# Kernel optimization log

Hardware: AMD Instinct MI355X
Metric: run time of the kernel (lower is better)

The kernel has to match this reference:

```python
import jax, jax.numpy as jnp
import numpy as np

DIM = 512
W = 64            # windowSize
R = 128           # receptiveSize
H = 8             # numHeads
HD = 64           # headDim
MAXD = W - 1 + (R - W) // 2  # maxDisparity = 95


def setup_inputs() -> dict:
    key = jax.random.key(0)
    ks = jax.random.split(key, 12)
    B_ = 512
    inp = {
        'x':  jax.random.normal(ks[0], (B_, 1 + W, DIM), jnp.float32),
        'x_': jax.random.normal(ks[1], (B_, 1 + R, DIM), jnp.float32),
        'mask_left':  jax.random.randint(ks[2], (4, 1 + W, 1 + R), 0, 2, jnp.int32),
        'mask_right': jax.random.randint(ks[3], (4, 1 + W, 1 + R), 0, 2, jnp.int32),
        'nW': 64,
        'rel_table': jax.random.normal(ks[4], (2 * MAXD + 1, H), jnp.float32) * 0.02,
        'cls_self':  jax.random.normal(ks[5], (1, H, 1, 1), jnp.float32) * 0.02,
        'cls_up':    jax.random.normal(ks[6], (1, H, 1, R), jnp.float32) * 0.02,
        'cls_down':  jax.random.normal(ks[7], (1, H, W, 1), jnp.float32) * 0.02,
        'Wq':  jax.random.normal(ks[8], (H * HD, DIM), jnp.float32) * 0.02,
        'bq':  jnp.zeros((H * HD,), jnp.float32),
        'Wkv': jax.random.normal(ks[9], (2 * H * HD, DIM), jnp.float32) * 0.02,
        'bkv': jnp.zeros((2 * H * HD,), jnp.float32),
        'Wp':  jax.random.normal(ks[10], (DIM, H * HD), jnp.float32) * 0.02,
        'bp':  jnp.zeros((DIM,), jnp.float32),
    }
    return inp


def _attention(x, x_, mask_left, mask_right, nW, rel_table, cls_self, cls_up,
               cls_down, Wq, bq, Wkv, bkv, Wp, bp):
    B_, n, C = x.shape   # n = 1+W
    m = x_.shape[1]      # m = 1+R
    B = B_ // nW
    scale = HD ** -0.5

    q = x @ Wq.T + bq                                  # (B_, n, H*HD)
    kv = x_ @ Wkv.T + bkv                              # (B_, m, 2*H*HD)
    k, v = jnp.split(kv, 2, axis=-1)
    q = q.reshape(B_, n, H, HD).transpose(0, 2, 1, 3)  # (B_, H, n, d)
    k = k.reshape(B_, m, H, HD).transpose(0, 2, 1, 3)
    v = v.reshape(B_, m, H, HD).transpose(0, 2, 1, 3)

    attn = jnp.einsum('bhnd,bhmd->bhnm', q, k) * scale  # (B_, H, n, m)

    # relative position bias gathered from the table
    coords = jnp.arange(W)[:, None] - (jnp.arange(R) - (R - W) // 2)[None, :] + MAXD
    rel_bias = rel_table[coords]                       # (W, R, H)
    rel_bias = rel_bias.transpose(2, 0, 1)             # (H, W, R)

    # assemble full (H, n, m) bias: cls-self | cls-up row ; cls-down col | rel body
    top = jnp.concatenate([cls_self[0], cls_up[0]], axis=2)       # (H, 1, 1+R)
    bot = jnp.concatenate([cls_down[0], rel_bias], axis=2)        # (H, W, 1+R)
    bias = jnp.concatenate([top, bot], axis=1)                    # (H, n, m)
    attn = attn + bias[None]

    # boundary-window masking
    mask_value = -jnp.finfo(attn.dtype).max
    attn = attn.reshape(B, nW, H, n, m)
    mc = min(mask_left.shape[0], nW)
    ml = mask_left[:mc][None, :, None]    # (1, mc, 1, n, m)
    mr = mask_right[-mc:][None, :, None]
    attn = attn.at[:, :mc].set(jnp.where(ml == 1, mask_value, attn[:, :mc]))
    attn = attn.at[:, nW - mc:].set(jnp.where(mr == 1, mask_value, attn[:, nW - mc:]))
    attn = attn.reshape(B_, H, n, m)

    attn = jax.nn.softmax(attn, axis=-1)
    out = jnp.einsum('bhnm,bhmd->bhnd', attn, v)       # (B_, H, n, d)
    out = out.transpose(0, 2, 1, 3).reshape(B_, n, H * HD)
    return out @ Wp.T + bp                             # (B_, n, C)


def reference(x, x_, mask_left, mask_right, nW, rel_table, cls_self, cls_up,
              cls_down, Wq, bq, Wkv, bkv, Wp, bp):
    return _attention(x, x_, mask_left, mask_right, nW, rel_table, cls_self,
                      cls_up, cls_down, Wq, bq, Wkv, bkv, Wp, bp)
```

## Files before the change

### kernel.cpp

```cpp
#include <hip/hip_runtime.h>
#include <float.h>

#define DIMC 512
#define WW 64
#define RR 128
#define NH 8
#define HDIM 64
#define NSEQ 65
#define MSEQ 129

typedef __attribute__((ext_vector_type(8))) short short8;
typedef __attribute__((ext_vector_type(4))) float f32x4;
typedef __attribute__((ext_vector_type(4))) unsigned int u32x4;
typedef __attribute__((ext_vector_type(4))) unsigned short u16x4;

typedef __attribute__((address_space(3))) unsigned int lds_uint;
typedef __attribute__((address_space(1))) unsigned int glob_uint;

__device__ __forceinline__ float asfloat(unsigned int u) { union { unsigned int i; float f; } v; v.i = u; return v.f; }
__device__ __forceinline__ unsigned int asuint(float f) { union { float f; unsigned int i; } v; v.f = f; return v.i; }
__device__ __forceinline__ unsigned short f2bf(float f) {
  unsigned int x = asuint(f);
  x += 0x7fffu + ((x >> 16) & 1u);
  return (unsigned short)(x >> 16);
}
__device__ __forceinline__ float bf2f(unsigned short b) { return asfloat(((unsigned int)b) << 16); }

__device__ __forceinline__ short8 ld_b64x2(const unsigned short* p) {
  typedef __attribute__((ext_vector_type(4))) short sh4;
  sh4 lo = *(const sh4*)p;
  sh4 hi = *(const sh4*)(p + 4);
  short8 r;
  r[0] = lo[0]; r[1] = lo[1]; r[2] = lo[2]; r[3] = lo[3];
  r[4] = hi[0]; r[5] = hi[1]; r[6] = hi[2]; r[7] = hi[3];
  return r;
}

__global__ void convert_f32_bf16(const float* __restrict__ s,
                                 unsigned short* __restrict__ d, long n4) {
  long stride = (long)gridDim.x * blockDim.x;
  for (long i = (long)blockIdx.x * blockDim.x + threadIdx.x; i < n4; i += stride) {
    f32x4 f = ((const f32x4*)s)[i];
    u16x4 o;
    o[0] = f2bf(f[0]); o[1] = f2bf(f[1]); o[2] = f2bf(f[2]); o[3] = f2bf(f[3]);
    ((u16x4*)d)[i] = o;
  }
}

template<int OUTBF>
__global__ __launch_bounds__(256)
void gemm_nt(const unsigned short* __restrict__ A, const unsigned short* __restrict__ Bw,
             const float* __restrict__ bias, void* __restrict__ Cout,
             long M, long N, long K, int gx) {
  __shared__ unsigned short As[128 * 64];
  __shared__ unsigned short Bs[128 * 64];
  const int nwg  = gridDim.x;
  const int orig = blockIdx.x;
  const int q8 = nwg >> 3, r8 = nwg & 7;
  const int xcd = orig & 7, sub = orig >> 3;
  const int wg = (xcd < r8 ? xcd * (q8 + 1) : r8 * (q8 + 1) + (xcd - r8) * q8) + sub;
  const long nBase = (long)(wg % gx) * 128;
  const long mBase = (long)(wg / gx) * 128;

  const int tid  = threadIdx.x;
  const int lane = tid & 63;
  const int wid  = tid >> 6;
  const int wr   = wid >> 1, wc = wid & 1;
  const int r15 = lane & 15;
  const int g16 = lane >> 4;

  f32x4 acc[4][4];
#pragma unroll
  for (int a = 0; a < 4; ++a)
#pragma unroll
    for (int b = 0; b < 4; ++b) acc[a][b] = (f32x4){0.f, 0.f, 0.f, 0.f};

  const int srow = tid >> 3;
  const int skb  = (tid & 7) * 8;

  for (long kt = 0; kt < K; kt += 64) {
    __syncthreads();
#pragma unroll
    for (int j = 0; j < 4; ++j) {
      long row = j * 32 + srow;
      const unsigned short* ga = A  + (mBase + row) * K + kt + skb;
      const unsigned short* gb = Bw + (nBase + row) * K + kt + skb;
      __builtin_amdgcn_global_load_lds((glob_uint*)ga, (lds_uint*)(As + (j * 256 + wid * 64) * 8), 16, 0, 0);
      __builtin_amdgcn_global_load_lds((glob_uint*)gb, (lds_uint*)(Bs + (j * 256 + wid * 64) * 8), 16, 0, 0);
    }
    __syncthreads();
#pragma unroll
    for (int kk = 0; kk < 64; kk += 32) {
      short8 af[4], bfr[4];
#pragma unroll
      for (int mi = 0; mi < 4; ++mi)
        af[mi] = *(const short8*)&As[(wr * 64 + mi * 16 + r15) * 64 + kk + g16 * 8];
#pragma unroll
      for (int ni = 0; ni < 4; ++ni)
        bfr[ni] = *(const short8*)&Bs[(wc * 64 + ni * 16 + r15) * 64 + kk + g16 * 8];
#pragma unroll
      for (int mi = 0; mi < 4; ++mi)
#pragma unroll
        for (int ni = 0; ni < 4; ++ni)
          acc[mi][ni] = __builtin_amdgcn_mfma_f32_16x16x32_bf16(af[mi], bfr[ni], acc[mi][ni], 0, 0, 0);
    }
  }

  float bv[4];
  long col[4];
#pragma unroll
  for (int ni = 0; ni < 4; ++ni) { col[ni] = nBase + wc * 64 + ni * 16 + r15; bv[ni] = bias[col[ni]]; }
#pragma unroll
  for (int mi = 0; mi < 4; ++mi) {
    long row0 = mBase + wr * 64 + mi * 16 + g16 * 4;
#pragma unroll
    for (int ni = 0; ni < 4; ++ni) {
#pragma unroll
      for (int v = 0; v < 4; ++v) {
        float val = acc[mi][ni][v] + bv[ni];
        long off = (row0 + v) * N + col[ni];
        if (OUTBF) ((unsigned short*)Cout)[off] = f2bf(val);
        else       ((float*)Cout)[off] = val;
      }
    }
  }
}

#define VT_OFF 0
#define VT_STR 140
#define K_OFF  (64 * VT_STR)
#define P_OFF  K_OFF
#define P_STR  136
#define SMEM_ELEMS (K_OFF + 80 * P_STR)

__global__ __launch_bounds__(256, 3)
void attn_mfma(const unsigned short* __restrict__ qb,
               const unsigned short* __restrict__ kvb,
               unsigned short* __restrict__ aob,
               const float* __restrict__ rel_table,
               const float* __restrict__ cls_self,
               const float* __restrict__ cls_up,
               const float* __restrict__ cls_down,
               const int* __restrict__ mask_left,
               const int* __restrict__ mask_right,
               const int* __restrict__ nWp, int mcL) {
  __shared__ unsigned short smem[SMEM_ELEMS];
  const int h   = blockIdx.x;
  const int b_  = blockIdx.y;
  const int tid = threadIdx.x, lane = tid & 63, wid = tid >> 6;
  const int r15 = lane & 15, g16 = lane >> 4;

  const int nW = nWp[0];
  const int w  = b_ % nW;
  const int mc = min(mcL, nW);
  const bool useL = (w < mc);
  const bool useR = (w >= nW - mc);
  const int wR = mcL - mc + (w - (nW - mc));

  const unsigned short* kgbase = kvb + (long)b_ * MSEQ * (2 * DIMC) + h * HDIM;
  const unsigned short* vgbase = kgbase + DIMC;
  const unsigned short* qgbase = qb  + (long)b_ * NSEQ * DIMC + h * HDIM;

  const int lr  = lane >> 3;
  const int lcs = ((lane & 7) ^ (lr & 7)) * 8;
#pragma unroll
  for (int j = 0; j < 4; ++j) {
    int chunk = j * 4 + wid;
    int gr = chunk * 8 + lr;
    __builtin_amdgcn_global_load_lds((glob_uint*)(kgbase + (long)gr * (2 * DIMC) + lcs),
                                     (lds_uint*)(smem + K_OFF + chunk * 512), 16, 0, 0);
  }
  if (wid == 0) {
    __builtin_amdgcn_global_load_lds((glob_uint*)(kgbase + (long)128 * (2 * DIMC) + lcs),
                                     (lds_uint*)(smem + K_OFF + 16 * 512), 16, 0, 0);
  }

  for (int it = 0; it < 5; ++it) {
    int idx = it * 256 + tid;
    if (idx < MSEQ * 8) {
      int c = idx >> 3, d0 = (idx & 7) * 8;
      u32x4 u = *(const u32x4*)(vgbase + (long)c * (2 * DIMC) + d0);
#pragma unroll
      for (int jj = 0; jj < 4; ++jj) {
        smem[VT_OFF + (d0 + 2 * jj) * VT_STR + c]     = (unsigned short)(u[jj] & 0xffffu);
        smem[VT_OFF + (d0 + 2 * jj + 1) * VT_STR + c] = (unsigned short)(u[jj] >> 16);
      }
    }
  }
  __syncthreads();

  f32x4 S[2][9];
  const int swz = (r15 & 7) << 3;
#pragma unroll
  for (int t = 0; t < 2; ++t) {
    if (t == 1 && wid != 0) continue;
    const int i0 = (t == 0 ? wid : 4) * 16;
    const int qrow = min(i0 + r15, NSEQ - 1);
    const unsigned short* qp = qgbase + (long)qrow * DIMC;
    short8 a0 = *(const short8*)(qp + g16 * 8);
    short8 a1 = *(const short8*)(qp + 32 + g16 * 8);
#pragma unroll
    for (int ni = 0; ni < 9; ++ni) {
      short8 b0 = *(const short8*)&smem[K_OFF + (ni * 16 + r15) * 64 + ((g16 * 8) ^ swz)];
      short8 b1 = *(const short8*)&smem[K_OFF + (ni * 16 + r15) * 64 + ((32 + g16 * 8) ^ swz)];
      f32x4 c = (f32x4){0.f, 0.f, 0.f, 0.f};
      c = __builtin_amdgcn_mfma_f32_16x16x32_bf16(a0, b0, c, 0, 0, 0);
      c = __builtin_amdgcn_mfma_f32_16x16x32_bf16(a1, b1, c, 0, 0, 0);
      S[t][ni] = c;
    }
  }

  float p128[2][4];
#pragma unroll
  for (int t = 0; t < 2; ++t) {
    if (t == 1 && wid != 0) continue;
    const int i0 = (t == 0 ? wid : 4) * 16;
#pragma unroll
    for (int v = 0; v < 4; ++v) {
      int row  = i0 + g16 * 4 + v;
      int rowb = min(row, NSEQ - 1);
#pragma unroll
      for (int ni = 0; ni < 9; ++ni) {
        int col = ni * 16 + r15;
        float val;
        if (col > 128) {
          val = -FLT_MAX;
        } else {
          float bias;
          if (row == 0) bias = (col == 0) ? cls_self[h] : cls_up[h * RR + col - 1];
          else bias = (col == 0) ? cls_down[h * WW + rowb - 1]
                                 : rel_table[min(rowb - col + 127, 190) * NH + h];
          val = S[t][ni][v] * 0.125f + bias;
          if (useL && mask_left[((long)w * NSEQ + rowb) * MSEQ + col])  val = -FLT_MAX;
          if (useR && mask_right[((long)wR * NSEQ + rowb) * MSEQ + col]) val = -FLT_MAX;
        }
        S[t][ni][v] = val;
      }
    }
#pragma unroll
    for (int v = 0; v < 4; ++v) {
      float m = S[t][0][v];
#pragma unroll
      for (int ni = 1; ni < 9; ++ni) m = fmaxf(m, S[t][ni][v]);
#pragma unroll
      for (int off = 1; off < 16; off <<= 1) m = fmaxf(m, __shfl_xor(m, off, 64));
      float sum = 0.f;
#pragma unroll
      for (int ni = 0; ni < 9; ++ni) {
        float p = __expf(S[t][ni][v] - m);
        S[t][ni][v] = p;
        sum += p;
      }
#pragma unroll
      for (int off = 1; off < 16; off <<= 1) sum += __shfl_xor(sum, off, 64);
      float inv = 1.0f / sum;
#pragma unroll
      for (int ni = 0; ni < 9; ++ni) S[t][ni][v] *= inv;
    }
#pragma unroll
    for (int v = 0; v < 4; ++v) p128[t][v] = S[t][8][v];
  }
  __syncthreads();

#pragma unroll
  for (int t = 0; t < 2; ++t) {
    if (t == 1 && wid != 0) continue;
    const int i0 = (t == 0 ? wid : 4) * 16;
#pragma unroll
    for (int ni = 0; ni < 8; ++ni)
#pragma unroll
      for (int v = 0; v < 4; ++v)
        smem[P_OFF + (i0 + g16 * 4 + v) * P_STR + ni * 16 + r15] = f2bf(S[t][ni][v]);
  }
  __syncthreads();

#pragma unroll
  for (int t = 0; t < 2; ++t) {
    if (t == 1 && wid != 0) continue;
    const int i0 = (t == 0 ? wid : 4) * 16;
    short8 pa[4];
#pragma unroll
    for (int kk = 0; kk < 4; ++kk)
      pa[kk] = *(const short8*)&smem[P_OFF + (i0 + r15) * P_STR + kk * 32 + g16 * 8];
    f32x4 acc[4];
#pragma unroll
    for (int nt = 0; nt < 4; ++nt) acc[nt] = (f32x4){0.f, 0.f, 0.f, 0.f};
#pragma unroll
    for (int nt = 0; nt < 4; ++nt)
#pragma unroll
      for (int kk = 0; kk < 4; ++kk) {
        short8 bv = ld_b64x2(&smem[VT_OFF + (nt * 16 + r15) * VT_STR + kk * 32 + g16 * 8]);
        acc[nt] = __builtin_amdgcn_mfma_f32_16x16x32_bf16(pa[kk], bv, acc[nt], 0, 0, 0);
      }
    float p1b[4];
#pragma unroll
    for (int v = 0; v < 4; ++v) p1b[v] = __shfl(p128[t][v], (lane & 48), 64);
#pragma unroll
    for (int nt = 0; nt < 4; ++nt) {
      float v128 = bf2f(smem[VT_OFF + (nt * 16 + r15) * VT_STR + 128]);
#pragma unroll
      for (int v = 0; v < 4; ++v) {
        int row = i0 + g16 * 4 + v;
        if (row < NSEQ) {
          float o = acc[nt][v] + p1b[v] * v128;
          aob[((long)b_ * NSEQ + row) * DIMC + h * HDIM + nt * 16 + r15] = f2bf(o);
        }
      }
    }
  }
}

extern "C" void kernel_launch(void* const* d_in, const int* in_sizes, int n_in,
                              void* d_out, int out_size, void* d_ws, size_t ws_size,
                              hipStream_t stream) {
  const float* x          = (const float*)d_in[0];
  const float* x_         = (const float*)d_in[1];
  const int*   mask_left  = (const int*)d_in[2];
  const int*   mask_right = (const int*)d_in[3];
  const int*   nWp        = (const int*)d_in[4];
  const float* rel_table  = (const float*)d_in[5];
  const float* cls_self   = (const float*)d_in[6];
  const float* cls_up     = (const float*)d_in[7];
  const float* cls_down   = (const float*)d_in[8];
  const float* Wq         = (const float*)d_in[9];
  const float* bq         = (const float*)d_in[10];
  const float* Wkv        = (const float*)d_in[11];
  const float* bkv        = (const float*)d_in[12];
  const float* Wp         = (const float*)d_in[13];
  const float* bp         = (const float*)d_in[14];

  const long B_  = in_sizes[0] / (NSEQ * DIMC);
  const int  mcL = in_sizes[2] / (NSEQ * MSEQ);
  const long Mq  = B_ * NSEQ;
  const long Mkv = B_ * MSEQ;

  unsigned short* xb    = (unsigned short*)d_ws;
  unsigned short* x_b   = xb    + Mq  * DIMC;
  unsigned short* wqb   = x_b   + Mkv * DIMC;
  unsigned short* wkvb  = wqb   + DIMC * DIMC;
  unsigned short* wpb   = wkvb  + 2 * DIMC * DIMC;
  unsigned short* qbuf  = wpb   + DIMC * DIMC;
  unsigned short* kvbuf = qbuf  + Mq  * DIMC;
  unsigned short* aob   = kvbuf + Mkv * 2 * DIMC;
  const size_t needed = (size_t)(Mq * DIMC * 3 + Mkv * DIMC * 3 + 4 * DIMC * DIMC) * 2;
  if (ws_size < needed) return;

  auto cv = [&](const float* s, unsigned short* d, long n) {
    long n4 = n / 4;
    int blocks = (int)((n4 + 255) / 256); if (blocks > 8192) blocks = 8192;
    convert_f32_bf16<<<blocks, 256, 0, stream>>>(s, d, n4);
  };
  cv(x,   xb,   Mq * DIMC);
  cv(x_,  x_b,  Mkv * DIMC);
  cv(Wq,  wqb,  (long)DIMC * DIMC);
  cv(Wkv, wkvb, 2L * DIMC * DIMC);
  cv(Wp,  wpb,  (long)DIMC * DIMC);

  {
    int gx = DIMC / 128, nwg = (int)(gx * (Mq / 128));
    gemm_nt<1><<<nwg, 256, 0, stream>>>(xb, wqb, bq, qbuf, Mq, DIMC, DIMC, gx);
  }
  {
    int gx = 2 * DIMC / 128, nwg = (int)(gx * (Mkv / 128));
    gemm_nt<1><<<nwg, 256, 0, stream>>>(x_b, wkvb, bkv, kvbuf, Mkv, 2 * DIMC, DIMC, gx);
  }

  attn_mfma<<<dim3(NH, (unsigned)B_), 256, 0, stream>>>(
      qbuf, kvbuf, aob, rel_table, cls_self, cls_up, cls_down,
      mask_left, mask_right, nWp, mcL);

  {
    int gx = DIMC / 128, nwg = (int)(gx * (Mq / 128));
    gemm_nt<0><<<nwg, 256, 0, stream>>>(aob, wpb, bp, d_out, Mq, DIMC, DIMC, gx);
  }
}
```

Measured before the change: 653.2 us.

## Replace tiled GEMM with persistent B-stationary GEMM streaming A from global

The 128x128 LDS-tiled GEMM is replaced by a persistent kernel. Each 512-thread block loads a full 128x512 weight slice into LDS once, using an XOR swizzle to avoid bank conflicts, then loops over 256-row M tiles. A fragments are read straight from global memory into registers with a one-step prefetch. The goal is to stop reloading weights for every output tile and to drop the per-K-tile LDS barriers. The costs are 128KB of LDS per block, which limits occupancy to one block per CU, and A reads that are duplicated across wave columns and exposed to global latency.

```diff
diff --git a/kernel.cpp b/kernel.cpp
--- a/kernel.cpp
+++ b/kernel.cpp
@@ -48,79 +48,92 @@
 }
 
 template<int OUTBF>
-__global__ __launch_bounds__(256)
-void gemm_nt(const unsigned short* __restrict__ A, const unsigned short* __restrict__ Bw,
-             const float* __restrict__ bias, void* __restrict__ Cout,
-             long M, long N, long K, int gx) {
-  __shared__ unsigned short As[128 * 64];
-  __shared__ unsigned short Bs[128 * 64];
-  const int nwg  = gridDim.x;
-  const int orig = blockIdx.x;
-  const int q8 = nwg >> 3, r8 = nwg & 7;
-  const int xcd = orig & 7, sub = orig >> 3;
-  const int wg = (xcd < r8 ? xcd * (q8 + 1) : r8 * (q8 + 1) + (xcd - r8) * q8) + sub;
-  const long nBase = (long)(wg % gx) * 128;
-  const long mBase = (long)(wg / gx) * 128;
-
-  const int tid  = threadIdx.x;
-  const int lane = tid & 63;
-  const int wid  = tid >> 6;
-  const int wr   = wid >> 1, wc = wid & 1;
-  const int r15 = lane & 15;
-  const int g16 = lane >> 4;
-
-  f32x4 acc[4][4];
-#pragma unroll
-  for (int a = 0; a < 4; ++a)
-#pragma unroll
-    for (int b = 0; b < 4; ++b) acc[a][b] = (f32x4){0.f, 0.f, 0.f, 0.f};
-
-  const int srow = tid >> 3;
-  const int skb  = (tid & 7) * 8;
-
-  for (long kt = 0; kt < K; kt += 64) {
-    __syncthreads();
-#pragma unroll
-    for (int j = 0; j < 4; ++j) {
-      long row = j * 32 + srow;
-      const unsigned short* ga = A  + (mBase + row) * K + kt + skb;
-      const unsigned short* gb = Bw + (nBase + row) * K + kt + skb;
-      __builtin_amdgcn_global_load_lds((glob_uint*)ga, (lds_uint*)(As + (j * 256 + wid * 64) * 8), 16, 0, 0);
-      __builtin_amdgcn_global_load_lds((glob_uint*)gb, (lds_uint*)(Bs + (j * 256 + wid * 64) * 8), 16, 0, 0);
-    }
-    __syncthreads();
-#pragma unroll
-    for (int kk = 0; kk < 64; kk += 32) {
-      short8 af[4], bfr[4];
+__global__ __launch_bounds__(512, 2)
+void gemm_bstat(const unsigned short* __restrict__ A, const unsigned short* __restrict__ Bw,
+                const float* __restrict__ bias, void* __restrict__ Cout,
+                long M, long N, int ncols , int mtiles ) {
+  __shared__ unsigned short Bs[128 * 512];
+  const int t    = threadIdx.x;
+  const int lane = t & 63, wid = t >> 6;
+  const int r15  = lane & 15, g16 = lane >> 4;
+  const int wm   = wid >> 1, wn = wid & 1;
+  const int npc  = 256 / ncols;
+  const int n    = blockIdx.x / npc;
+  const int mset = blockIdx.x % npc;
+  const long nBase = (long)n * 128;
+
+  {
+    const int k8d = t & 63, rsub = t >> 6;
+#pragma unroll
+    for (int i = 0; i < 16; ++i) {
+      int row = i * 8 + rsub;
+      const unsigned short* gb = Bw + (nBase + row) * DIMC + ((k8d ^ rsub) * 8);
+      __builtin_amdgcn_global_load_lds((glob_uint*)gb,
+                                       (lds_uint*)(Bs + row * DIMC + k8d * 8), 16, 0, 0);
+    }
+  }
+
+  float bv[4];
+  long colv[4];
+#pragma unroll
+  for (int ni = 0; ni < 4; ++ni) {
+    colv[ni] = nBase + wn * 64 + ni * 16 + r15;
+    bv[ni] = bias[colv[ni]];
+  }
+  __syncthreads();
+
+  for (int mt = mset; mt < mtiles; mt += npc) {
+    const long mBase = (long)mt * 256;
+    const unsigned short* ap[4];
+#pragma unroll
+    for (int mi = 0; mi < 4; ++mi)
+      ap[mi] = A + (mBase + wm * 64 + mi * 16 + r15) * DIMC + g16 * 8;
+
+    f32x4 acc[4][4];
+#pragma unroll
+    for (int a = 0; a < 4; ++a)
+#pragma unroll
+      for (int b = 0; b < 4; ++b) acc[a][b] = (f32x4){0.f, 0.f, 0.f, 0.f};
+
+    short8 a_n[4];
+#pragma unroll
+    for (int mi = 0; mi < 4; ++mi) a_n[mi] = *(const short8*)(ap[mi]);
+
+#pragma unroll
+    for (int kk = 0; kk < 16; ++kk) {
+      short8 a_c[4];
+#pragma unroll
+      for (int mi = 0; mi < 4; ++mi) a_c[mi] = a_n[mi];
+      if (kk < 15) {
+#pragma unroll
+        for (int mi = 0; mi < 4; ++mi) a_n[mi] = *(const short8*)(ap[mi] + (kk + 1) * 32);
+      }
+      short8 bf[4];
+#pragma unroll
+      for (int ni = 0; ni < 4; ++ni) {
+        int row = wn * 64 + ni * 16 + r15;
+        int k8r = (kk * 4 + g16) ^ (r15 & 7);
+        bf[ni] = *(const short8*)&Bs[row * DIMC + k8r * 8];
+      }
 #pragma unroll
       for (int mi = 0; mi < 4; ++mi)
-        af[mi] = *(const short8*)&As[(wr * 64 + mi * 16 + r15) * 64 + kk + g16 * 8];
-#pragma unroll
-      for (int ni = 0; ni < 4; ++ni)
-        bfr[ni] = *(const short8*)&Bs[(wc * 64 + ni * 16 + r15) * 64 + kk + g16 * 8];
-#pragma unroll
-      for (int mi = 0; mi < 4; ++mi)
 #pragma unroll
         for (int ni = 0; ni < 4; ++ni)
-          acc[mi][ni] = __builtin_amdgcn_mfma_f32_16x16x32_bf16(af[mi], bfr[ni], acc[mi][ni], 0, 0, 0);
-    }
-  }
-
-  float bv[4];
-  long col[4];
-#pragma unroll
-  for (int ni = 0; ni < 4; ++ni) { col[ni] = nBase + wc * 64 + ni * 16 + r15; bv[ni] = bias[col[ni]]; }
-#pragma unroll
-  for (int mi = 0; mi < 4; ++mi) {
-    long row0 = mBase + wr * 64 + mi * 16 + g16 * 4;
-#pragma unroll
-    for (int ni = 0; ni < 4; ++ni) {
-#pragma unroll
-      for (int v = 0; v < 4; ++v) {
-        float val = acc[mi][ni][v] + bv[ni];
-        long off = (row0 + v) * N + col[ni];
-        if (OUTBF) ((unsigned short*)Cout)[off] = f2bf(val);
-        else       ((float*)Cout)[off] = val;
+          acc[mi][ni] = __builtin_amdgcn_mfma_f32_16x16x32_bf16(a_c[mi], bf[ni], acc[mi][ni], 0, 0, 0);
+    }
+
+#pragma unroll
+    for (int mi = 0; mi < 4; ++mi) {
+      long row0 = mBase + wm * 64 + mi * 16 + g16 * 4;
+#pragma unroll
+      for (int ni = 0; ni < 4; ++ni) {
+#pragma unroll
+        for (int v = 0; v < 4; ++v) {
+          float val = acc[mi][ni][v] + bv[ni];
+          long off = (row0 + v) * N + colv[ni];
+          if (OUTBF) ((unsigned short*)Cout)[off] = f2bf(val);
+          else       ((float*)Cout)[off] = val;
+        }
       }
     }
   }
@@ -356,21 +369,15 @@
   cv(Wkv, wkvb, 2L * DIMC * DIMC);
   cv(Wp,  wpb,  (long)DIMC * DIMC);
 
-  {
-    int gx = DIMC / 128, nwg = (int)(gx * (Mq / 128));
-    gemm_nt<1><<<nwg, 256, 0, stream>>>(xb, wqb, bq, qbuf, Mq, DIMC, DIMC, gx);
-  }
-  {
-    int gx = 2 * DIMC / 128, nwg = (int)(gx * (Mkv / 128));
-    gemm_nt<1><<<nwg, 256, 0, stream>>>(x_b, wkvb, bkv, kvbuf, Mkv, 2 * DIMC, DIMC, gx);
-  }
+  gemm_bstat<1><<<256, 512, 0, stream>>>(xb, wqb, bq, qbuf,
+                                         Mq, DIMC, DIMC / 128, (int)(Mq / 256));
+  gemm_bstat<1><<<256, 512, 0, stream>>>(x_b, wkvb, bkv, kvbuf,
+                                         Mkv, 2 * DIMC, 2 * DIMC / 128, (int)(Mkv / 256));
 
   attn_mfma<<<dim3(NH, (unsigned)B_), 256, 0, stream>>>(
       qbuf, kvbuf, aob, rel_table, cls_self, cls_up, cls_down,
       mask_left, mask_right, nWp, mcL);
 
-  {
-    int gx = DIMC / 128, nwg = (int)(gx * (Mq / 128));
-    gemm_nt<0><<<nwg, 256, 0, stream>>>(aob, wpb, bp, d_out, Mq, DIMC, DIMC, gx);
-  }
-}
+  gemm_bstat<0><<<256, 512, 0, stream>>>(aob, wpb, bp, d_out,
+                                         Mq, DIMC, DIMC / 128, (int)(Mq / 256));
+}
```

Result: slower. 958.7 us (+46.8%).
